# Kernel tuning notes

Hardware: AMD Instinct MI355X
Metric: run time of the kernel (lower is better)

Reference implementation:

```python
import jax, jax.numpy as jnp
import numpy as np

NEG_SLOPE = 0.2
NUM_GRAPHS = 512


def gat_conv(x, W, att_src, att_dst, bias, src, dst, n):
    """Single-head PyG GATConv (concat=True trivially, heads=1).
    x: [N, Fin], W: [Fin, Fout], att_*: [Fout], bias: [Fout].
    src/dst: [E] int32/64 (self-loops already appended).
    """
    h = x @ W                               # [N, Fout]
    a_s = h @ att_src                       # [N]
    a_d = h @ att_dst                       # [N]
    e = a_s[src] + a_d[dst]                 # [E]
    e = jnp.where(e >= 0, e, NEG_SLOPE * e)  # LeakyReLU
    # numerically stable edge-softmax grouped by destination node
    m = jax.ops.segment_max(e, dst, num_segments=n)          # [N]
    w = jnp.exp(e - m[dst])                                   # [E]
    denom = jax.ops.segment_sum(w, dst, num_segments=n)      # [N]
    alpha = w / denom[dst]                                    # [E]
    out = jax.ops.segment_sum(alpha[:, None] * h[src], dst, num_segments=n)
    return out + bias


def setup_inputs() -> dict:
    key = jax.random.key(0)
    ks = jax.random.split(key, 12)
    N, E, FIN, H = 50000, 800000, 768, 64
    x = jax.random.normal(ks[0], (N, FIN), dtype=jnp.float32)
    edge_index = jax.random.randint(ks[1], (2, E), 0, N, dtype=jnp.int64)
    batch = jnp.sort(jax.random.randint(ks[2], (N,), 0, NUM_GRAPHS, dtype=jnp.int64))
    def glorot(k, shape):
        lim = np.sqrt(6.0 / (shape[0] + shape[-1]))
        return jax.random.uniform(k, shape, jnp.float32, -lim, lim)
    return {
        "x": x, "edge_index": edge_index, "batch": batch,
        "W1": glorot(ks[3], (FIN, H)),
        "att_src1": glorot(ks[4], (H,)), "att_dst1": glorot(ks[5], (H,)),
        "b1": jnp.zeros((H,), jnp.float32),
        "W2": glorot(ks[6], (H, H)),
        "att_src2": glorot(ks[7], (H,)), "att_dst2": glorot(ks[8], (H,)),
        "b2": jnp.zeros((H,), jnp.float32),
        "Wlin": glorot(ks[9], (H, 2)),
        "blin": jnp.zeros((2,), jnp.float32),
    }


def reference(x, edge_index, batch, W1, att_src1, att_dst1, b1,
              W2, att_src2, att_dst2, b2, Wlin, blin):
    n = x.shape[0]
    loops = jnp.arange(n, dtype=edge_index.dtype)
    src = jnp.concatenate([edge_index[0], loops])  # add_self_loops=True
    dst = jnp.concatenate([edge_index[1], loops])
    h = gat_conv(x, W1, att_src1, att_dst1, b1, src, dst, n)
    h = jax.nn.relu(h)
    h = gat_conv(h, W2, att_src2, att_dst2, b2, src, dst, n)
    h = jax.nn.relu(h)
    # global_mean_pool
    sums = jax.ops.segment_sum(h, batch, num_segments=NUM_GRAPHS)     # [G, H]
    cnt = jax.ops.segment_sum(jnp.ones((n,), h.dtype), batch, num_segments=NUM_GRAPHS)
    pooled = sums / jnp.maximum(cnt, 1.0)[:, None]
    return pooled @ Wlin + blin
```

## Files before the change

kernel.cpp:

```cpp
#include <hip/hip_runtime.h>

#define NEG_SLOPE 0.2f
#define NGRAPHS 512

typedef short short8 __attribute__((ext_vector_type(8)));
typedef float f32x4 __attribute__((ext_vector_type(4)));

__device__ __forceinline__ float wave_reduce_sum(float v) {
#pragma unroll
    for (int off = 32; off > 0; off >>= 1) v += __shfl_xor(v, off, 64);
    return v;
}
__device__ __forceinline__ float wave_reduce_max(float v) {
#pragma unroll
    for (int off = 32; off > 0; off >>= 1) v = fmaxf(v, __shfl_xor(v, off, 64));
    return v;
}
__device__ __forceinline__ unsigned short f2bf(float f) {
    unsigned u = __float_as_uint(f);
    u += 0x7FFFu + ((u >> 16) & 1u);
    return (unsigned short)(u >> 16);
}

__global__ __launch_bounds__(256) void convert_w(const float* __restrict__ W,
                                                 unsigned short* __restrict__ Wt,
                                                 int K) {
    int n = blockIdx.x;
    for (int k = threadIdx.x; k < K; k += 256)
        Wt[(size_t)n * K + k] = f2bf(W[(size_t)k * 64 + n]);
}

__global__ __launch_bounds__(256) void gemm_att_mfma(
    const float* __restrict__ A, const unsigned short* __restrict__ Wt, int M, int K,
    float* __restrict__ h, const float* __restrict__ att_s,
    const float* __restrict__ att_d, float* __restrict__ a_s,
    float* __restrict__ a_d) {
    __shared__ unsigned short As[64][72];
    const int tid = threadIdx.x;
    const int w = tid >> 6, l = tid & 63, m = l & 15, q = l >> 4;
    const int row0 = blockIdx.x * 64;
    f32x4 acc0 = {0.f, 0.f, 0.f, 0.f}, acc1 = acc0, acc2 = acc0, acc3 = acc0;
    const int sr = tid >> 2, sc = tid & 3;
    const int grow = row0 + sr;
    const bool rok = grow < M;
    if (!rok) {
#pragma unroll
        for (int j = 0; j < 16; ++j) As[sr][sc * 16 + j] = 0;
    }
    const float* Ap = A + (size_t)grow * K + sc * 16;

    for (int k0 = 0; k0 < K; k0 += 64) {
        if (rok) {
            const float4* p = (const float4*)(Ap + k0);
            float4 f0 = p[0], f1 = p[1], f2 = p[2], f3 = p[3];
            unsigned short t[16] = {
                f2bf(f0.x), f2bf(f0.y), f2bf(f0.z), f2bf(f0.w),
                f2bf(f1.x), f2bf(f1.y), f2bf(f1.z), f2bf(f1.w),
                f2bf(f2.x), f2bf(f2.y), f2bf(f2.z), f2bf(f2.w),
                f2bf(f3.x), f2bf(f3.y), f2bf(f3.z), f2bf(f3.w)};
            *(uint4*)&As[sr][sc * 16] = *(uint4*)&t[0];
            *(uint4*)&As[sr][sc * 16 + 8] = *(uint4*)&t[8];
        }
        __syncthreads();
        const unsigned short* arow = &As[w * 16 + m][0];
        const unsigned short* brow = Wt + (size_t)m * K + k0;
#pragma unroll
        for (int kk = 0; kk < 2; ++kk) {
            short8 av = *(const short8*)(arow + kk * 32 + q * 8);
            const unsigned short* bp = brow + kk * 32 + q * 8;
            acc0 = __builtin_amdgcn_mfma_f32_16x16x32_bf16(
                av, *(const short8*)(bp), acc0, 0, 0, 0);
            acc1 = __builtin_amdgcn_mfma_f32_16x16x32_bf16(
                av, *(const short8*)(bp + (size_t)16 * K), acc1, 0, 0, 0);
            acc2 = __builtin_amdgcn_mfma_f32_16x16x32_bf16(
                av, *(const short8*)(bp + (size_t)32 * K), acc2, 0, 0, 0);
            acc3 = __builtin_amdgcn_mfma_f32_16x16x32_bf16(
                av, *(const short8*)(bp + (size_t)48 * K), acc3, 0, 0, 0);
        }
        __syncthreads();
    }
    float as0 = att_s[m], as1 = att_s[16 + m], as2 = att_s[32 + m], as3 = att_s[48 + m];
    float ad0 = att_d[m], ad1 = att_d[16 + m], ad2 = att_d[32 + m], ad3 = att_d[48 + m];
    const int rowb = row0 + w * 16 + q * 4;
#pragma unroll
    for (int r = 0; r < 4; ++r) {
        int row = rowb + r;
        float v0 = acc0[r], v1 = acc1[r], v2 = acc2[r], v3 = acc3[r];
        if (row < M) {
            float* hp = h + (size_t)row * 64 + m;
            hp[0] = v0; hp[16] = v1; hp[32] = v2; hp[48] = v3;
        }
        float hs = v0 * as0 + v1 * as1 + v2 * as2 + v3 * as3;
        float hd = v0 * ad0 + v1 * ad1 + v2 * ad2 + v3 * ad3;
#pragma unroll
        for (int off = 1; off < 16; off <<= 1) {
            hs += __shfl_xor(hs, off, 64);
            hd += __shfl_xor(hd, off, 64);
        }
        if (m == 0 && row < M) { a_s[row] = hs; a_d[row] = hd; }
    }
}

__global__ __launch_bounds__(256) void gemm64s(const float* __restrict__ A,
                                               const float* __restrict__ B,
                                               float* __restrict__ C, int M, int K,
                                               const float* __restrict__ att_s,
                                               const float* __restrict__ att_d,
                                               float* __restrict__ a_s,
                                               float* __restrict__ a_d) {
    __shared__ float As[16][64];
    __shared__ float Bs[16][64];
    const int tid = threadIdx.x;
    const int tx = tid & 15;
    const int ty = tid >> 4;
    const int row0 = blockIdx.x * 64;
    float acc[4][4] = {};
    const int la_row = tid >> 2;
    const int la_col = (tid & 3) * 4;
    const int lb_row = tid >> 4;
    const int lb_col = (tid & 15) * 4;

    for (int k0 = 0; k0 < K; k0 += 16) {
        int ar = row0 + la_row;
        float4 av = make_float4(0.f, 0.f, 0.f, 0.f);
        if (ar < M) av = *(const float4*)(A + (size_t)ar * K + k0 + la_col);
        As[la_col + 0][la_row] = av.x;
        As[la_col + 1][la_row] = av.y;
        As[la_col + 2][la_row] = av.z;
        As[la_col + 3][la_row] = av.w;
        *(float4*)&Bs[lb_row][lb_col] =
            *(const float4*)(B + (size_t)(k0 + lb_row) * 64 + lb_col);
        __syncthreads();
#pragma unroll
        for (int k = 0; k < 16; ++k) {
            float4 a4 = *(float4*)&As[k][ty * 4];
            float4 b4 = *(float4*)&Bs[k][tx * 4];
            acc[0][0] += a4.x * b4.x; acc[0][1] += a4.x * b4.y;
            acc[0][2] += a4.x * b4.z; acc[0][3] += a4.x * b4.w;
            acc[1][0] += a4.y * b4.x; acc[1][1] += a4.y * b4.y;
            acc[1][2] += a4.y * b4.z; acc[1][3] += a4.y * b4.w;
            acc[2][0] += a4.z * b4.x; acc[2][1] += a4.z * b4.y;
            acc[2][2] += a4.z * b4.z; acc[2][3] += a4.z * b4.w;
            acc[3][0] += a4.w * b4.x; acc[3][1] += a4.w * b4.y;
            acc[3][2] += a4.w * b4.z; acc[3][3] += a4.w * b4.w;
        }
        __syncthreads();
    }
    float asv[4], adv[4];
#pragma unroll
    for (int j = 0; j < 4; ++j) {
        asv[j] = att_s[tx * 4 + j];
        adv[j] = att_d[tx * 4 + j];
    }
#pragma unroll
    for (int i = 0; i < 4; ++i) {
        int row = row0 + ty * 4 + i;
        if (row < M) {
            float4 v = make_float4(acc[i][0], acc[i][1], acc[i][2], acc[i][3]);
            *(float4*)(C + (size_t)row * 64 + tx * 4) = v;
        }
        float hs = acc[i][0] * asv[0] + acc[i][1] * asv[1] +
                   acc[i][2] * asv[2] + acc[i][3] * asv[3];
        float hd = acc[i][0] * adv[0] + acc[i][1] * adv[1] +
                   acc[i][2] * adv[2] + acc[i][3] * adv[3];
#pragma unroll
        for (int off = 1; off < 16; off <<= 1) {
            hs += __shfl_xor(hs, off, 64);
            hd += __shfl_xor(hd, off, 64);
        }
        if (tx == 0 && row < M) { a_s[row] = hs; a_d[row] = hd; }
    }
}

__device__ __forceinline__ void edge_sd(const int* __restrict__ ei, int E, int e,
                                        int& s, int& d) {
    if (e < E) { s = ei[e]; d = ei[E + e]; }
    else { s = d = e - E; }
}

__global__ __launch_bounds__(256) void hist_kernel(const int* __restrict__ ei, int E,
                                                   int ET, int* __restrict__ counts) {
    int e = blockIdx.x * 256 + threadIdx.x;
    if (e >= ET) return;
    int s, d;
    edge_sd(ei, E, e, s, d);
    atomicAdd(counts + d, 1);
}

__global__ __launch_bounds__(256) void scan_sum(const int* __restrict__ counts,
                                                int* __restrict__ blk_sum, int N,
                                                int CH) {
    __shared__ int wsum[4];
    const int tid = threadIdx.x, lane = tid & 63, wid = tid >> 6;
    const int b = blockIdx.x;
    int begin = b * CH, endi = min(begin + CH, N);
    int s = 0;
    for (int i = begin + tid; i < endi; i += 256) s += counts[i];
#pragma unroll
    for (int off = 32; off > 0; off >>= 1) s += __shfl_xor(s, off, 64);
    if (lane == 0) wsum[wid] = s;
    __syncthreads();
    if (tid == 0) blk_sum[b] = wsum[0] + wsum[1] + wsum[2] + wsum[3];
}

__global__ __launch_bounds__(64) void scan_blk(int* __restrict__ blk_sum,
                                               int* __restrict__ row_ptr, int N,
                                               int nb) {
    int t = threadIdx.x;
    int v = (t < nb) ? blk_sum[t] : 0;
    int sv = v;
#pragma unroll
    for (int off = 1; off < 64; off <<= 1) {
        int u = __shfl_up(sv, off, 64);
        if (t >= off) sv += u;
    }
    if (t < nb) blk_sum[t] = sv - v;
    if (t == nb - 1) row_ptr[N] = sv;
}

__global__ __launch_bounds__(256) void scan_local(const int* __restrict__ counts,
                                                  const int* __restrict__ blk_off,
                                                  int* __restrict__ row_ptr,
                                                  int* __restrict__ next_, int N,
                                                  int CH) {
    __shared__ int wsum[4];
    __shared__ int ctot;
    const int tid = threadIdx.x, lane = tid & 63, wid = tid >> 6;
    const int b = blockIdx.x;
    int begin = b * CH, endi = min(begin + CH, N);
    int carry = blk_off[b];
    for (int base = begin; base < endi; base += 256) {
        int i = base + tid;
        int v = (i < endi) ? counts[i] : 0;
        int sv = v;
#pragma unroll
        for (int off = 1; off < 64; off <<= 1) {
            int u = __shfl_up(sv, off, 64);
            if (lane >= off) sv += u;
        }
        if (lane == 63) wsum[wid] = sv;
        __syncthreads();
        if (tid == 0) {
            int a = 0;
#pragma unroll
            for (int j = 0; j < 4; ++j) { int u = wsum[j]; wsum[j] = a; a += u; }
            ctot = a;
        }
        __syncthreads();
        int excl = carry + wsum[wid] + sv - v;
        if (i < endi) { row_ptr[i] = excl; next_[i] = excl; }
        carry += ctot;
        __syncthreads();
    }
}

__global__ __launch_bounds__(256) void fill_kernel(const int* __restrict__ ei, int E,
                                                   int ET, int* __restrict__ next,
                                                   int* __restrict__ srcs) {
    int e = blockIdx.x * 256 + threadIdx.x;
    if (e >= ET) return;
    int s, d;
    edge_sd(ei, E, e, s, d);
    int pos = atomicAdd(next + d, 1);
    srcs[pos] = s;
}

__global__ __launch_bounds__(256) void gat_agg_kernel(const int* __restrict__ row_ptr,
                                                      const int* __restrict__ srcs,
                                                      const float* __restrict__ a_s,
                                                      const float* __restrict__ a_d,
                                                      const float* __restrict__ h,
                                                      const float* __restrict__ bias,
                                                      float* __restrict__ out, int N) {
    int n = blockIdx.x * 4 + (threadIdx.x >> 6);
    int lane = threadIdx.x & 63;
    if (n >= N) return;
    const int start = row_ptr[n];
    const int deg = row_ptr[n + 1] - start;
    const float adn = a_d[n];

    if (deg <= 64) {
        int sl = 0;
        float v = -1e30f;
        if (lane < deg) {
            sl = srcs[start + lane];
            float t = a_s[sl] + adn;
            v = (t >= 0.f) ? t : NEG_SLOPE * t;
        }
        float m = wave_reduce_max(v);
        float wl = (lane < deg) ? __expf(v - m) : 0.f;
        float l = wave_reduce_sum(wl);
        wl *= (1.f / l);

        const int eq = lane >> 4, fq = lane & 15;
        float ax = 0.f, ay = 0.f, az = 0.f, aw = 0.f;
        for (int j = 0; j < deg; j += 4) {
            int idx = j + eq;
            bool ok = idx < deg;
            int ii = ok ? idx : 0;
            float a = __shfl(wl, ii, 64);
            int s = __shfl(sl, ii, 64);
            if (!ok) a = 0.f;
            const float4 hv = *(const float4*)(h + (size_t)s * 64 + fq * 4);
            ax += a * hv.x; ay += a * hv.y; az += a * hv.z; aw += a * hv.w;
        }
#pragma unroll
        for (int off = 16; off <= 32; off <<= 1) {
            ax += __shfl_xor(ax, off, 64);
            ay += __shfl_xor(ay, off, 64);
            az += __shfl_xor(az, off, 64);
            aw += __shfl_xor(aw, off, 64);
        }
        if (eq == 0) {
            const float4 bv = *(const float4*)(bias + fq * 4);
            float4 o;
            o.x = ax + bv.x; o.y = ay + bv.y; o.z = az + bv.z; o.w = aw + bv.w;
            o.x = o.x > 0.f ? o.x : 0.f;
            o.y = o.y > 0.f ? o.y : 0.f;
            o.z = o.z > 0.f ? o.z : 0.f;
            o.w = o.w > 0.f ? o.w : 0.f;
            *(float4*)(out + (size_t)n * 64 + fq * 4) = o;
        }
        return;
    }

    const int end = start + deg;
    float m = -1e30f;
    for (int i = start + lane; i < end; i += 64) {
        float v = a_s[srcs[i]] + adn;
        v = (v >= 0.f) ? v : NEG_SLOPE * v;
        m = fmaxf(m, v);
    }
    m = wave_reduce_max(m);
    float l = 0.f;
    for (int i = start + lane; i < end; i += 64) {
        float v = a_s[srcs[i]] + adn;
        v = (v >= 0.f) ? v : NEG_SLOPE * v;
        l += __expf(v - m);
    }
    l = wave_reduce_sum(l);
    const float inv_den = 1.f / l;
    float acc = 0.f;
    for (int c = start; c < end; c += 64) {
        int cl = end - c;
        if (cl > 64) cl = 64;
        int sl = 0;
        float wl = 0.f;
        if (c + lane < end) {
            sl = srcs[c + lane];
            float v = a_s[sl] + adn;
            v = (v >= 0.f) ? v : NEG_SLOPE * v;
            wl = __expf(v - m) * inv_den;
        }
        for (int j = 0; j < cl; ++j) {
            float wj = __shfl(wl, j, 64);
            int sj = __shfl(sl, j, 64);
            acc += wj * h[(size_t)sj * 64 + lane];
        }
    }
    float o = acc + bias[lane];
    out[(size_t)n * 64 + lane] = o > 0.f ? o : 0.f;
}

__global__ __launch_bounds__(256) void graph_bounds(const int* __restrict__ batch,
                                                    int* __restrict__ gstart, int N) {
    int g = blockIdx.x * 256 + threadIdx.x;
    if (g > NGRAPHS) return;
    int lo = 0, hi = N;
    while (lo < hi) {
        int mid = (lo + hi) >> 1;
        if (batch[mid] < g) lo = mid + 1; else hi = mid;
    }
    gstart[g] = lo;
}

__global__ __launch_bounds__(256) void pool_final(const float* __restrict__ x,
                                                  const int* __restrict__ gstart,
                                                  const float* __restrict__ Wlin,
                                                  const float* __restrict__ blin,
                                                  float* __restrict__ out) {
    __shared__ float red[4][64];
    const int g = blockIdx.x;
    const int lane = threadIdx.x & 63, w = threadIdx.x >> 6;
    const int s = gstart[g], e = gstart[g + 1];
    float acc = 0.f;
    for (int n = s + w; n < e; n += 4) acc += x[(size_t)n * 64 + lane];
    red[w][lane] = acc;
    __syncthreads();
    if (w == 0) {
        float p = red[0][lane] + red[1][lane] + red[2][lane] + red[3][lane];
        int c = e - s;
        p /= (float)(c > 1 ? c : 1);
        float o0 = wave_reduce_sum(p * Wlin[lane * 2 + 0]);
        float o1 = wave_reduce_sum(p * Wlin[lane * 2 + 1]);
        if (lane == 0) {
            out[g * 2 + 0] = o0 + blin[0];
            out[g * 2 + 1] = o1 + blin[1];
        }
    }
}

extern "C" void kernel_launch(void* const* d_in, const int* in_sizes, int n_in,
                              void* d_out, int out_size, void* d_ws, size_t ws_size,
                              hipStream_t stream) {
    const float* x    = (const float*)d_in[0];
    const int*   ei   = (const int*)d_in[1];
    const int*   batch= (const int*)d_in[2];
    const float* W1   = (const float*)d_in[3];
    const float* as1  = (const float*)d_in[4];
    const float* ad1  = (const float*)d_in[5];
    const float* b1   = (const float*)d_in[6];
    const float* W2   = (const float*)d_in[7];
    const float* as2  = (const float*)d_in[8];
    const float* ad2  = (const float*)d_in[9];
    const float* b2   = (const float*)d_in[10];
    const float* Wlin = (const float*)d_in[11];
    const float* blin = (const float*)d_in[12];
    float* out = (float*)d_out;

    const int FIN = 768;
    const int N  = in_sizes[0] / FIN;
    const int E  = in_sizes[1] / 2;
    const int ET = E + N;
    const size_t N64 = (size_t)N * 64;
    const int NB = 64;
    const int CH = (N + NB - 1) / NB;

    float* ws     = (float*)d_ws;
    float* hbuf   = ws;
    float* x1     = hbuf + N64;
    float* x2     = x1 + N64;
    float* a_s    = x2 + N64;
    float* a_d    = a_s + N;
    int* counts   = (int*)(a_d + N);
    int* row_ptr  = counts + N;
    int* next     = row_ptr + N + 1;
    int* blk_sum  = next + N;
    int* gstart   = blk_sum + 64;
    int* srcs     = gstart + NGRAPHS + 1;
    uintptr_t wtp = (uintptr_t)(srcs + ET);
    wtp = (wtp + 15) & ~(uintptr_t)15;
    unsigned short* Wt1 = (unsigned short*)wtp;
    unsigned short* Wt2 = Wt1 + (size_t)64 * FIN;

    const int nEdgeBlk  = (ET + 255) / 256;
    const int nWaveBlkN = (N + 3) / 4;
    const int nGemmBlk  = (N + 63) / 64;

    hipMemsetAsync(counts, 0, (size_t)N * sizeof(int), stream);

    convert_w<<<64, 256, 0, stream>>>(W1, Wt1, FIN);
    convert_w<<<64, 256, 0, stream>>>(W2, Wt2, 64);
    graph_bounds<<<(NGRAPHS + 256) / 256, 256, 0, stream>>>(batch, gstart, N);

    hist_kernel<<<nEdgeBlk, 256, 0, stream>>>(ei, E, ET, counts);
    scan_sum<<<NB, 256, 0, stream>>>(counts, blk_sum, N, CH);
    scan_blk<<<1, 64, 0, stream>>>(blk_sum, row_ptr, N, NB);
    scan_local<<<NB, 256, 0, stream>>>(counts, blk_sum, row_ptr, next, N, CH);
    fill_kernel<<<nEdgeBlk, 256, 0, stream>>>(ei, E, ET, next, srcs);

    gemm_att_mfma<<<nGemmBlk, 256, 0, stream>>>(x, Wt1, N, FIN, hbuf, as1, ad1,
                                                a_s, a_d);
    gat_agg_kernel<<<nWaveBlkN, 256, 0, stream>>>(row_ptr, srcs, a_s, a_d, hbuf,
                                                  b1, x1, N);

    gemm64s<<<nGemmBlk, 256, 0, stream>>>(x1, W2, hbuf, N, 64, as2, ad2, a_s, a_d);
    gat_agg_kernel<<<nWaveBlkN, 256, 0, stream>>>(row_ptr, srcs, a_s, a_d, hbuf,
                                                  b2, x2, N);

    pool_final<<<NGRAPHS, 256, 0, stream>>>(x2, gstart, Wlin, blin, out);
}
```

Before: 468.5 us.

## Fuse setup kernels, overlap edge fill with GEMM1, use MFMA bf16 for layer-2 GEMM

Merges the weight conversion, graph-bounds search and degree histogram into one launch. Folds the CSR fill pass into the first GEMM launch as extra blocks so the two run concurrently. GEMM1 now stages 256-wide K chunks in shared memory, giving fewer barriers. The first aggregation writes a bf16 copy of x1, which a new MFMA-based layer-2 GEMM consumes instead of the fp32 scalar GEMM. This cuts launch count and layer-2 traffic, at the cost of bf16 rounding of the layer-1 activations and a larger shared-memory footprint in GEMM1.

```diff
diff --git a/kernel.cpp b/kernel.cpp
--- a/kernel.cpp
+++ b/kernel.cpp
@@ -22,169 +22,45 @@
     return (unsigned short)(u >> 16);
 }
 
-__global__ __launch_bounds__(256) void convert_w(const float* __restrict__ W,
-                                                 unsigned short* __restrict__ Wt,
-                                                 int K) {
-    int n = blockIdx.x;
-    for (int k = threadIdx.x; k < K; k += 256)
-        Wt[(size_t)n * K + k] = f2bf(W[(size_t)k * 64 + n]);
-}
-
-__global__ __launch_bounds__(256) void gemm_att_mfma(
-    const float* __restrict__ A, const unsigned short* __restrict__ Wt, int M, int K,
-    float* __restrict__ h, const float* __restrict__ att_s,
-    const float* __restrict__ att_d, float* __restrict__ a_s,
-    float* __restrict__ a_d) {
-    __shared__ unsigned short As[64][72];
-    const int tid = threadIdx.x;
-    const int w = tid >> 6, l = tid & 63, m = l & 15, q = l >> 4;
-    const int row0 = blockIdx.x * 64;
-    f32x4 acc0 = {0.f, 0.f, 0.f, 0.f}, acc1 = acc0, acc2 = acc0, acc3 = acc0;
-    const int sr = tid >> 2, sc = tid & 3;
-    const int grow = row0 + sr;
-    const bool rok = grow < M;
-    if (!rok) {
-#pragma unroll
-        for (int j = 0; j < 16; ++j) As[sr][sc * 16 + j] = 0;
-    }
-    const float* Ap = A + (size_t)grow * K + sc * 16;
-
-    for (int k0 = 0; k0 < K; k0 += 64) {
-        if (rok) {
-            const float4* p = (const float4*)(Ap + k0);
-            float4 f0 = p[0], f1 = p[1], f2 = p[2], f3 = p[3];
-            unsigned short t[16] = {
-                f2bf(f0.x), f2bf(f0.y), f2bf(f0.z), f2bf(f0.w),
-                f2bf(f1.x), f2bf(f1.y), f2bf(f1.z), f2bf(f1.w),
-                f2bf(f2.x), f2bf(f2.y), f2bf(f2.z), f2bf(f2.w),
-                f2bf(f3.x), f2bf(f3.y), f2bf(f3.z), f2bf(f3.w)};
-            *(uint4*)&As[sr][sc * 16] = *(uint4*)&t[0];
-            *(uint4*)&As[sr][sc * 16 + 8] = *(uint4*)&t[8];
-        }
-        __syncthreads();
-        const unsigned short* arow = &As[w * 16 + m][0];
-        const unsigned short* brow = Wt + (size_t)m * K + k0;
-#pragma unroll
-        for (int kk = 0; kk < 2; ++kk) {
-            short8 av = *(const short8*)(arow + kk * 32 + q * 8);
-            const unsigned short* bp = brow + kk * 32 + q * 8;
-            acc0 = __builtin_amdgcn_mfma_f32_16x16x32_bf16(
-                av, *(const short8*)(bp), acc0, 0, 0, 0);
-            acc1 = __builtin_amdgcn_mfma_f32_16x16x32_bf16(
-                av, *(const short8*)(bp + (size_t)16 * K), acc1, 0, 0, 0);
-            acc2 = __builtin_amdgcn_mfma_f32_16x16x32_bf16(
-                av, *(const short8*)(bp + (size_t)32 * K), acc2, 0, 0, 0);
-            acc3 = __builtin_amdgcn_mfma_f32_16x16x32_bf16(
-                av, *(const short8*)(bp + (size_t)48 * K), acc3, 0, 0, 0);
-        }
-        __syncthreads();
-    }
-    float as0 = att_s[m], as1 = att_s[16 + m], as2 = att_s[32 + m], as3 = att_s[48 + m];
-    float ad0 = att_d[m], ad1 = att_d[16 + m], ad2 = att_d[32 + m], ad3 = att_d[48 + m];
-    const int rowb = row0 + w * 16 + q * 4;
-#pragma unroll
-    for (int r = 0; r < 4; ++r) {
-        int row = rowb + r;
-        float v0 = acc0[r], v1 = acc1[r], v2 = acc2[r], v3 = acc3[r];
-        if (row < M) {
-            float* hp = h + (size_t)row * 64 + m;
-            hp[0] = v0; hp[16] = v1; hp[32] = v2; hp[48] = v3;
-        }
-        float hs = v0 * as0 + v1 * as1 + v2 * as2 + v3 * as3;
-        float hd = v0 * ad0 + v1 * ad1 + v2 * ad2 + v3 * ad3;
-#pragma unroll
-        for (int off = 1; off < 16; off <<= 1) {
-            hs += __shfl_xor(hs, off, 64);
-            hd += __shfl_xor(hd, off, 64);
-        }
-        if (m == 0 && row < M) { a_s[row] = hs; a_d[row] = hd; }
-    }
-}
-
-__global__ __launch_bounds__(256) void gemm64s(const float* __restrict__ A,
-                                               const float* __restrict__ B,
-                                               float* __restrict__ C, int M, int K,
-                                               const float* __restrict__ att_s,
-                                               const float* __restrict__ att_d,
-                                               float* __restrict__ a_s,
-                                               float* __restrict__ a_d) {
-    __shared__ float As[16][64];
-    __shared__ float Bs[16][64];
-    const int tid = threadIdx.x;
-    const int tx = tid & 15;
-    const int ty = tid >> 4;
-    const int row0 = blockIdx.x * 64;
-    float acc[4][4] = {};
-    const int la_row = tid >> 2;
-    const int la_col = (tid & 3) * 4;
-    const int lb_row = tid >> 4;
-    const int lb_col = (tid & 15) * 4;
-
-    for (int k0 = 0; k0 < K; k0 += 16) {
-        int ar = row0 + la_row;
-        float4 av = make_float4(0.f, 0.f, 0.f, 0.f);
-        if (ar < M) av = *(const float4*)(A + (size_t)ar * K + k0 + la_col);
-        As[la_col + 0][la_row] = av.x;
-        As[la_col + 1][la_row] = av.y;
-        As[la_col + 2][la_row] = av.z;
-        As[la_col + 3][la_row] = av.w;
-        *(float4*)&Bs[lb_row][lb_col] =
-            *(const float4*)(B + (size_t)(k0 + lb_row) * 64 + lb_col);
-        __syncthreads();
-#pragma unroll
-        for (int k = 0; k < 16; ++k) {
-            float4 a4 = *(float4*)&As[k][ty * 4];
-            float4 b4 = *(float4*)&Bs[k][tx * 4];
-            acc[0][0] += a4.x * b4.x; acc[0][1] += a4.x * b4.y;
-            acc[0][2] += a4.x * b4.z; acc[0][3] += a4.x * b4.w;
-            acc[1][0] += a4.y * b4.x; acc[1][1] += a4.y * b4.y;
-            acc[1][2] += a4.y * b4.z; acc[1][3] += a4.y * b4.w;
-            acc[2][0] += a4.z * b4.x; acc[2][1] += a4.z * b4.y;
-            acc[2][2] += a4.z * b4.z; acc[2][3] += a4.z * b4.w;
-            acc[3][0] += a4.w * b4.x; acc[3][1] += a4.w * b4.y;
-            acc[3][2] += a4.w * b4.z; acc[3][3] += a4.w * b4.w;
-        }
-        __syncthreads();
-    }
-    float asv[4], adv[4];
-#pragma unroll
-    for (int j = 0; j < 4; ++j) {
-        asv[j] = att_s[tx * 4 + j];
-        adv[j] = att_d[tx * 4 + j];
-    }
-#pragma unroll
-    for (int i = 0; i < 4; ++i) {
-        int row = row0 + ty * 4 + i;
-        if (row < M) {
-            float4 v = make_float4(acc[i][0], acc[i][1], acc[i][2], acc[i][3]);
-            *(float4*)(C + (size_t)row * 64 + tx * 4) = v;
-        }
-        float hs = acc[i][0] * asv[0] + acc[i][1] * asv[1] +
-                   acc[i][2] * asv[2] + acc[i][3] * asv[3];
-        float hd = acc[i][0] * adv[0] + acc[i][1] * adv[1] +
-                   acc[i][2] * adv[2] + acc[i][3] * adv[3];
-#pragma unroll
-        for (int off = 1; off < 16; off <<= 1) {
-            hs += __shfl_xor(hs, off, 64);
-            hd += __shfl_xor(hd, off, 64);
-        }
-        if (tx == 0 && row < M) { a_s[row] = hs; a_d[row] = hd; }
-    }
-}
-
 __device__ __forceinline__ void edge_sd(const int* __restrict__ ei, int E, int e,
                                         int& s, int& d) {
     if (e < E) { s = ei[e]; d = ei[E + e]; }
     else { s = d = e - E; }
 }
 
-__global__ __launch_bounds__(256) void hist_kernel(const int* __restrict__ ei, int E,
-                                                   int ET, int* __restrict__ counts) {
-    int e = blockIdx.x * 256 + threadIdx.x;
-    if (e >= ET) return;
-    int s, d;
-    edge_sd(ei, E, e, s, d);
-    atomicAdd(counts + d, 1);
+__global__ __launch_bounds__(256) void setup_hist(
+    const int* __restrict__ ei, int E, int ET, int* __restrict__ counts,
+    int nEdgeBlk, const float* __restrict__ W1, unsigned short* __restrict__ Wt1,
+    int K1, const float* __restrict__ W2, unsigned short* __restrict__ Wt2,
+    const int* __restrict__ batch, int* __restrict__ gstart, int N) {
+    const int b = blockIdx.x, tid = threadIdx.x;
+    if (b < nEdgeBlk) {
+        int e = b * 256 + tid;
+        if (e >= ET) return;
+        int s, d;
+        edge_sd(ei, E, e, s, d);
+        atomicAdd(counts + d, 1);
+    } else if (b < nEdgeBlk + 64) {
+        int n = b - nEdgeBlk;
+        for (int k = tid; k < K1; k += 256)
+            Wt1[(size_t)n * K1 + k] = f2bf(W1[(size_t)k * 64 + n]);
+    } else if (b == nEdgeBlk + 64) {
+#pragma unroll
+        for (int i = 0; i < 16; ++i) {
+            int idx = tid + i * 256;
+            int n = idx >> 6, k = idx & 63;
+            Wt2[n * 64 + k] = f2bf(W2[k * 64 + n]);
+        }
+    } else {
+        for (int g = tid; g <= NGRAPHS; g += 256) {
+            int lo = 0, hi = N;
+            while (lo < hi) {
+                int mid = (lo + hi) >> 1;
+                if (batch[mid] < g) lo = mid + 1; else hi = mid;
+            }
+            gstart[g] = lo;
+        }
+    }
 }
 
 __global__ __launch_bounds__(256) void scan_sum(const int* __restrict__ counts,
@@ -254,24 +130,142 @@
     }
 }
 
-__global__ __launch_bounds__(256) void fill_kernel(const int* __restrict__ ei, int E,
-                                                   int ET, int* __restrict__ next,
-                                                   int* __restrict__ srcs) {
-    int e = blockIdx.x * 256 + threadIdx.x;
-    if (e >= ET) return;
-    int s, d;
-    edge_sd(ei, E, e, s, d);
-    int pos = atomicAdd(next + d, 1);
-    srcs[pos] = s;
-}
-
-__global__ __launch_bounds__(256) void gat_agg_kernel(const int* __restrict__ row_ptr,
-                                                      const int* __restrict__ srcs,
-                                                      const float* __restrict__ a_s,
-                                                      const float* __restrict__ a_d,
-                                                      const float* __restrict__ h,
-                                                      const float* __restrict__ bias,
-                                                      float* __restrict__ out, int N) {
+__global__ __launch_bounds__(256) void gemm1_fill(
+    const float* __restrict__ A, const unsigned short* __restrict__ Wt, int M, int K,
+    float* __restrict__ h, const float* __restrict__ att_s,
+    const float* __restrict__ att_d, float* __restrict__ a_s,
+    float* __restrict__ a_d, int nGemm, const int* __restrict__ ei, int E, int ET,
+    int* __restrict__ next_, int* __restrict__ srcs) {
+    __shared__ unsigned short As[64][264];
+    const int tid = threadIdx.x;
+    if (blockIdx.x >= nGemm) {
+        int e = (blockIdx.x - nGemm) * 256 + tid;
+        if (e >= ET) return;
+        int s, d;
+        edge_sd(ei, E, e, s, d);
+        int pos = atomicAdd(next_ + d, 1);
+        srcs[pos] = s;
+        return;
+    }
+    const int w = tid >> 6, l = tid & 63, m = l & 15, q = l >> 4;
+    const int row0 = blockIdx.x * 64;
+    f32x4 acc0 = {0.f, 0.f, 0.f, 0.f}, acc1 = acc0, acc2 = acc0, acc3 = acc0;
+    const int sr = tid >> 2, sc = tid & 3;
+    const int grow = row0 + sr;
+    const bool rok = grow < M;
+    if (!rok) {
+#pragma unroll
+        for (int u = 0; u < 8; ++u)
+            *(uint4*)&As[sr][sc * 64 + u * 8] = make_uint4(0, 0, 0, 0);
+    }
+    const float* Ap = A + (size_t)grow * K + sc * 64;
+
+    for (int c = 0; c < 3; ++c) {
+        if (rok) {
+            for (int u = 0; u < 4; ++u) {
+                const float4* p = (const float4*)(Ap + c * 256 + u * 16);
+                float4 f0 = p[0], f1 = p[1], f2 = p[2], f3 = p[3];
+                unsigned short t[16] = {
+                    f2bf(f0.x), f2bf(f0.y), f2bf(f0.z), f2bf(f0.w),
+                    f2bf(f1.x), f2bf(f1.y), f2bf(f1.z), f2bf(f1.w),
+                    f2bf(f2.x), f2bf(f2.y), f2bf(f2.z), f2bf(f2.w),
+                    f2bf(f3.x), f2bf(f3.y), f2bf(f3.z), f2bf(f3.w)};
+                *(uint4*)&As[sr][sc * 64 + u * 16] = *(uint4*)&t[0];
+                *(uint4*)&As[sr][sc * 64 + u * 16 + 8] = *(uint4*)&t[8];
+            }
+        }
+        __syncthreads();
+        const unsigned short* arow = &As[w * 16 + m][0];
+        const unsigned short* brow = Wt + (size_t)m * K + c * 256;
+#pragma unroll
+        for (int ks = 0; ks < 8; ++ks) {
+            short8 av = *(const short8*)(arow + ks * 32 + q * 8);
+            const unsigned short* bp = brow + ks * 32 + q * 8;
+            acc0 = __builtin_amdgcn_mfma_f32_16x16x32_bf16(
+                av, *(const short8*)(bp), acc0, 0, 0, 0);
+            acc1 = __builtin_amdgcn_mfma_f32_16x16x32_bf16(
+                av, *(const short8*)(bp + (size_t)16 * K), acc1, 0, 0, 0);
+            acc2 = __builtin_amdgcn_mfma_f32_16x16x32_bf16(
+                av, *(const short8*)(bp + (size_t)32 * K), acc2, 0, 0, 0);
+            acc3 = __builtin_amdgcn_mfma_f32_16x16x32_bf16(
+                av, *(const short8*)(bp + (size_t)48 * K), acc3, 0, 0, 0);
+        }
+        __syncthreads();
+    }
+    float as0 = att_s[m], as1 = att_s[16 + m], as2 = att_s[32 + m], as3 = att_s[48 + m];
+    float ad0 = att_d[m], ad1 = att_d[16 + m], ad2 = att_d[32 + m], ad3 = att_d[48 + m];
+    const int rowb = row0 + w * 16 + q * 4;
+#pragma unroll
+    for (int r = 0; r < 4; ++r) {
+        int row = rowb + r;
+        float v0 = acc0[r], v1 = acc1[r], v2 = acc2[r], v3 = acc3[r];
+        if (row < M) {
+            float* hp = h + (size_t)row * 64 + m;
+            hp[0] = v0; hp[16] = v1; hp[32] = v2; hp[48] = v3;
+        }
+        float hs = v0 * as0 + v1 * as1 + v2 * as2 + v3 * as3;
+        float hd = v0 * ad0 + v1 * ad1 + v2 * ad2 + v3 * ad3;
+#pragma unroll
+        for (int off = 1; off < 16; off <<= 1) {
+            hs += __shfl_xor(hs, off, 64);
+            hd += __shfl_xor(hd, off, 64);
+        }
+        if (m == 0 && row < M) { a_s[row] = hs; a_d[row] = hd; }
+    }
+}
+
+__global__ __launch_bounds__(256) void gemm2_mfma(
+    const unsigned short* __restrict__ Ab, const unsigned short* __restrict__ Wt2,
+    int M, float* __restrict__ h, const float* __restrict__ att_s,
+    const float* __restrict__ att_d, float* __restrict__ a_s,
+    float* __restrict__ a_d) {
+    const int tid = threadIdx.x;
+    const int w = tid >> 6, l = tid & 63, m = l & 15, q = l >> 4;
+    const int row0 = blockIdx.x * 64;
+    const int r = row0 + w * 16 + m;
+    short8 av0 = {0, 0, 0, 0, 0, 0, 0, 0}, av1 = av0;
+    if (r < M) {
+        av0 = *(const short8*)(Ab + (size_t)r * 64 + q * 8);
+        av1 = *(const short8*)(Ab + (size_t)r * 64 + 32 + q * 8);
+    }
+    f32x4 acc0 = {0.f, 0.f, 0.f, 0.f}, acc1 = acc0, acc2 = acc0, acc3 = acc0;
+    const unsigned short* bp = Wt2 + (size_t)m * 64 + q * 8;
+    acc0 = __builtin_amdgcn_mfma_f32_16x16x32_bf16(av0, *(const short8*)(bp), acc0, 0, 0, 0);
+    acc0 = __builtin_amdgcn_mfma_f32_16x16x32_bf16(av1, *(const short8*)(bp + 32), acc0, 0, 0, 0);
+    acc1 = __builtin_amdgcn_mfma_f32_16x16x32_bf16(av0, *(const short8*)(bp + 16 * 64), acc1, 0, 0, 0);
+    acc1 = __builtin_amdgcn_mfma_f32_16x16x32_bf16(av1, *(const short8*)(bp + 16 * 64 + 32), acc1, 0, 0, 0);
+    acc2 = __builtin_amdgcn_mfma_f32_16x16x32_bf16(av0, *(const short8*)(bp + 32 * 64), acc2, 0, 0, 0);
+    acc2 = __builtin_amdgcn_mfma_f32_16x16x32_bf16(av1, *(const short8*)(bp + 32 * 64 + 32), acc2, 0, 0, 0);
+    acc3 = __builtin_amdgcn_mfma_f32_16x16x32_bf16(av0, *(const short8*)(bp + 48 * 64), acc3, 0, 0, 0);
+    acc3 = __builtin_amdgcn_mfma_f32_16x16x32_bf16(av1, *(const short8*)(bp + 48 * 64 + 32), acc3, 0, 0, 0);
+
+    float as0 = att_s[m], as1 = att_s[16 + m], as2 = att_s[32 + m], as3 = att_s[48 + m];
+    float ad0 = att_d[m], ad1 = att_d[16 + m], ad2 = att_d[32 + m], ad3 = att_d[48 + m];
+    const int rowb = row0 + w * 16 + q * 4;
+#pragma unroll
+    for (int rr = 0; rr < 4; ++rr) {
+        int row = rowb + rr;
+        float v0 = acc0[rr], v1 = acc1[rr], v2 = acc2[rr], v3 = acc3[rr];
+        if (row < M) {
+            float* hp = h + (size_t)row * 64 + m;
+            hp[0] = v0; hp[16] = v1; hp[32] = v2; hp[48] = v3;
+        }
+        float hs = v0 * as0 + v1 * as1 + v2 * as2 + v3 * as3;
+        float hd = v0 * ad0 + v1 * ad1 + v2 * ad2 + v3 * ad3;
+#pragma unroll
+        for (int off = 1; off < 16; off <<= 1) {
+            hs += __shfl_xor(hs, off, 64);
+            hd += __shfl_xor(hd, off, 64);
+        }
+        if (m == 0 && row < M) { a_s[row] = hs; a_d[row] = hd; }
+    }
+}
+
+__global__ __launch_bounds__(256) void gat_agg_kernel(
+    const int* __restrict__ row_ptr, const int* __restrict__ srcs,
+    const float* __restrict__ a_s, const float* __restrict__ a_d,
+    const float* __restrict__ h, const float* __restrict__ bias,
+    float* __restrict__ out, unsigned short* __restrict__ outb, int N) {
     int n = blockIdx.x * 4 + (threadIdx.x >> 6);
     int lane = threadIdx.x & 63;
     if (n >= N) return;
@@ -319,7 +313,11 @@
             o.y = o.y > 0.f ? o.y : 0.f;
             o.z = o.z > 0.f ? o.z : 0.f;
             o.w = o.w > 0.f ? o.w : 0.f;
-            *(float4*)(out + (size_t)n * 64 + fq * 4) = o;
+            if (out) *(float4*)(out + (size_t)n * 64 + fq * 4) = o;
+            if (outb) {
+                unsigned short t[4] = {f2bf(o.x), f2bf(o.y), f2bf(o.z), f2bf(o.w)};
+                *(uint2*)(outb + (size_t)n * 64 + fq * 4) = *(uint2*)t;
+            }
         }
         return;
     }
@@ -359,19 +357,9 @@
         }
     }
     float o = acc + bias[lane];
-    out[(size_t)n * 64 + lane] = o > 0.f ? o : 0.f;
-}
-
-__global__ __launch_bounds__(256) void graph_bounds(const int* __restrict__ batch,
-                                                    int* __restrict__ gstart, int N) {
-    int g = blockIdx.x * 256 + threadIdx.x;
-    if (g > NGRAPHS) return;
-    int lo = 0, hi = N;
-    while (lo < hi) {
-        int mid = (lo + hi) >> 1;
-        if (batch[mid] < g) lo = mid + 1; else hi = mid;
-    }
-    gstart[g] = lo;
+    o = o > 0.f ? o : 0.f;
+    if (out) out[(size_t)n * 64 + lane] = o;
+    if (outb) outb[(size_t)n * 64 + lane] = f2bf(o);
 }
 
 __global__ __launch_bounds__(256) void pool_final(const float* __restrict__ x,
@@ -428,8 +416,7 @@
 
     float* ws     = (float*)d_ws;
     float* hbuf   = ws;
-    float* x1     = hbuf + N64;
-    float* x2     = x1 + N64;
+    float* x2     = hbuf + N64;
     float* a_s    = x2 + N64;
     float* a_d    = a_s + N;
     int* counts   = (int*)(a_d + N);
@@ -442,6 +429,7 @@
     wtp = (wtp + 15) & ~(uintptr_t)15;
     unsigned short* Wt1 = (unsigned short*)wtp;
     unsigned short* Wt2 = Wt1 + (size_t)64 * FIN;
+    unsigned short* x1b = Wt2 + (size_t)64 * 64;
 
     const int nEdgeBlk  = (ET + 255) / 256;
     const int nWaveBlkN = (N + 3) / 4;
@@ -449,24 +437,21 @@
 
     hipMemsetAsync(counts, 0, (size_t)N * sizeof(int), stream);
 
-    convert_w<<<64, 256, 0, stream>>>(W1, Wt1, FIN);
-    convert_w<<<64, 256, 0, stream>>>(W2, Wt2, 64);
-    graph_bounds<<<(NGRAPHS + 256) / 256, 256, 0, stream>>>(batch, gstart, N);
-
-    hist_kernel<<<nEdgeBlk, 256, 0, stream>>>(ei, E, ET, counts);
+    setup_hist<<<nEdgeBlk + 66, 256, 0, stream>>>(ei, E, ET, counts, nEdgeBlk,
+                                                  W1, Wt1, FIN, W2, Wt2,
+                                                  batch, gstart, N);
     scan_sum<<<NB, 256, 0, stream>>>(counts, blk_sum, N, CH);
     scan_blk<<<1, 64, 0, stream>>>(blk_sum, row_ptr, N, NB);
     scan_local<<<NB, 256, 0, stream>>>(counts, blk_sum, row_ptr, next, N, CH);
-    fill_kernel<<<nEdgeBlk, 256, 0, stream>>>(ei, E, ET, next, srcs);
-
-    gemm_att_mfma<<<nGemmBlk, 256, 0, stream>>>(x, Wt1, N, FIN, hbuf, as1, ad1,
-                                                a_s, a_d);
+
+    gemm1_fill<<<nGemmBlk + nEdgeBlk, 256, 0, stream>>>(
+        x, Wt1, N, FIN, hbuf, as1, ad1, a_s, a_d, nGemmBlk, ei, E, ET, next, srcs);
     gat_agg_kernel<<<nWaveBlkN, 256, 0, stream>>>(row_ptr, srcs, a_s, a_d, hbuf,
-                                                  b1, x1, N);
-
-    gemm64s<<<nGemmBlk, 256, 0, stream>>>(x1, W2, hbuf, N, 64, as2, ad2, a_s, a_d);
+                                                  b1, nullptr, x1b, N);
+
+    gemm2_mfma<<<nGemmBlk, 256, 0, stream>>>(x1b, Wt2, N, hbuf, as2, ad2, a_s, a_d);
     gat_agg_kernel<<<nWaveBlkN, 256, 0, stream>>>(row_ptr, srcs, a_s, a_d, hbuf,
-                                                  b2, x2, N);
+                                                  b2, x2, nullptr, N);
 
     pool_final<<<NGRAPHS, 256, 0, stream>>>(x2, gstart, Wlin, blin, out);
 }
```

Measured after the change: 444.0 us. 1.06x faster.
